# Kernel optimization log

Hardware: AMD Instinct MI355X
Metric: run time of the kernel (lower is better)

## Reference

```python
import jax, jax.numpy as jnp
import numpy as np

IGNORE_INDEX = -100


def setup_inputs() -> dict:
    key = jax.random.key(0)
    k1, k2, k3 = jax.random.split(key, 3)
    B, S, D, V = 2, 4096, 2048, 32000
    outputs = jax.random.normal(k1, (B, S, D), dtype=jnp.float32)
    # LM-head weight, nn.Linear convention: [vocab, embed_dim], scaled like typical init
    weight = jax.random.normal(k2, (V, D), dtype=jnp.float32) * (D ** -0.5)
    targets = jax.random.randint(k3, (B, S), 0, V, dtype=jnp.int64)
    return {"outputs": outputs, "weight": weight, "targets": targets}


def reference(outputs, weight, targets):
    # Flatten tokens: [B, S, D] -> [N, D], [B, S] -> [N]
    D = outputs.shape[-1]
    x = outputs.reshape(-1, D)            # [N, D]
    t = targets.reshape(-1)               # [N]
    # Fused linear projection: logits [N, V]
    logits = jnp.einsum("nd,vd->nv", x, weight)
    logp = jax.nn.log_softmax(logits, axis=-1)
    valid = t != IGNORE_INDEX
    safe_t = jnp.where(valid, t, 0)
    # Gather target log-prob per token
    nll = -jnp.take_along_axis(logp, safe_t[:, None], axis=1)[:, 0]  # [N]
    n_valid = jnp.maximum(jnp.sum(valid.astype(nll.dtype)), 1.0)
    loss = jnp.sum(jnp.where(valid, nll, 0.0)) / n_valid
    return loss
```

## Files before the change

kernel.cpp:

```cpp
#include <hip/hip_runtime.h>
#include <hip/hip_bf16.h>
#include <math.h>

#define IGNORE_INDEX (-100)

typedef __attribute__((ext_vector_type(4))) float f32x4;
typedef __attribute__((ext_vector_type(2))) long lx2;

static const int NTOK = 2 * 4096;
static const int DIM  = 2048;
static const int VOC  = 32000;
static const int BM = 256, BN = 256;
static const int KS = 64;
static const int NPH = DIM / KS;
static const int NVT = VOC / BN;
static const int MT  = NTOK / BM;
static const float WSCALE = 16.0f;


__device__ inline void gload_lds16(const void* g, void* l) {
  __builtin_amdgcn_global_load_lds(
      (const __attribute__((address_space(1))) void*)g,
      (__attribute__((address_space(3))) void*)l,
      16, 0, 0);
}


__global__ void cast_f32_fp8(const float* __restrict__ in,
                             unsigned char* __restrict__ out, long n8, float scale) {
  long i0 = (long)blockIdx.x * blockDim.x + threadIdx.x;
  long stride = (long)gridDim.x * blockDim.x;
  for (long i = i0; i < n8; i += stride) {
    const float4* p = (const float4*)(in + i * 8);
    float4 a = p[0], b = p[1];
    int lo = __builtin_amdgcn_cvt_pk_fp8_f32(a.x * scale, a.y * scale, 0, false);
    lo = __builtin_amdgcn_cvt_pk_fp8_f32(a.z * scale, a.w * scale, lo, true);
    int hi = __builtin_amdgcn_cvt_pk_fp8_f32(b.x * scale, b.y * scale, 0, false);
    hi = __builtin_amdgcn_cvt_pk_fp8_f32(b.z * scale, b.w * scale, hi, true);
    int2 o; o.x = lo; o.y = hi;
    *(int2*)(out + i * 8) = o;
  }
}


#define VM8  asm volatile("s_waitcnt vmcnt(8)" ::: "memory")
#define VM4  asm volatile("s_waitcnt vmcnt(4)" ::: "memory")
#define VM0  asm volatile("s_waitcnt vmcnt(0)" ::: "memory")
#define BARRIER asm volatile("s_barrier" ::: "memory")
#define LGKM0 asm volatile("s_waitcnt lgkmcnt(0)" ::: "memory")

#define MM2(ii, jj, AR, BR) do { \
  acc[ii][jj] = __builtin_amdgcn_mfma_f32_16x16x32_fp8_fp8(AR[0], BR[0], acc[ii][jj], 0, 0, 0); \
  acc[ii][jj] = __builtin_amdgcn_mfma_f32_16x16x32_fp8_fp8(AR[1], BR[1], acc[ii][jj], 0, 0, 0); \
} while (0)

__launch_bounds__(512, 2)
__global__ void lce_gemm(const unsigned char* __restrict__ xq,
                         const unsigned char* __restrict__ wq,
                         float* __restrict__ pmax, float* __restrict__ psum) {
  extern __shared__ char smem[];
  char* smA = smem;
  char* smB = smem + 65536;

  const int nwg = NVT * MT;
  const int cpx = nwg >> 3;
  const int bid = blockIdx.x;
  const int swz = (bid & 7) * cpx + (bid >> 3);
  const int vt = swz / MT;
  const int mt = swz % MT;
  const int m0 = mt * BM;
  const int v0 = vt * BN;

  const int tid = threadIdx.x;
  const int lane = tid & 63;
  const int w = tid >> 6;
  const int wr = w >> 2, wc = w & 3;
  const int li = lane & 15, lg = lane >> 4;

  f32x4 acc[8][4];
  const f32x4 z = {0.f, 0.f, 0.f, 0.f};
#pragma unroll
  for (int i = 0; i < 8; ++i)
#pragma unroll
    for (int j = 0; j < 4; ++j) acc[i][j] = z;

  const unsigned char* aS0 = xq + (long)(m0 + 2 * w * 16 + li) * DIM + lg * 16;
  const unsigned char* aS1 = xq + (long)(m0 + (2 * w + 1) * 16 + li) * DIM + lg * 16;
  const unsigned char* bS0 = wq + (long)(v0 + 2 * w * 16 + li) * DIM + lg * 16;
  const unsigned char* bS1 = wq + (long)(v0 + (2 * w + 1) * 16 + li) * DIM + lg * 16;
  char* stA = smA + 2 * w * 1024;
  char* stB = smB + 2 * w * 1024;

  const char* aRd = smA + wr * 8192 + lane * 16;
  const char* bRd = smB + wc * 4096 + lane * 16;

#pragma unroll
  for (int s = 0; s < 3; ++s) {
    gload_lds16(aS0, stA + s * 16384);        aS0 += KS;
    gload_lds16(aS1, stA + s * 16384 + 1024); aS1 += KS;
    gload_lds16(bS0, stB + s * 16384);        bS0 += KS;
    gload_lds16(bS1, stB + s * 16384 + 1024); bS1 += KS;
  }
  VM8;
  BARRIER;

#pragma unroll 1
  for (int n = 0; n < NPH; ++n) {
    const int slot = n & 3;
    const int dst = (n + 3) & 3;
    const char* Ab = aRd + slot * 16384;
    const char* Bb = bRd + slot * 16384;
    const bool stg = (n < NPH - 3);

    lx2 B0 = *(const lx2*)(Bb);
    lx2 B1 = *(const lx2*)(Bb + 1024);
    lx2 B2 = *(const lx2*)(Bb + 2048);
    lx2 B3 = *(const lx2*)(Bb + 3072);
    lx2 A0 = *(const lx2*)(Ab);
    lx2 A1 = *(const lx2*)(Ab + 1024);
    if (stg) { gload_lds16(aS0, stA + dst * 16384); aS0 += KS; }
    BARRIER; LGKM0;
    __builtin_amdgcn_s_setprio(1);
    MM2(0, 0, A0, B0); MM2(0, 1, A0, B1); MM2(0, 2, A0, B2); MM2(0, 3, A0, B3);
    MM2(1, 0, A1, B0); MM2(1, 1, A1, B1); MM2(1, 2, A1, B2); MM2(1, 3, A1, B3);
    __builtin_amdgcn_s_setprio(0);
    BARRIER;

    A0 = *(const lx2*)(Ab + 2048);
    A1 = *(const lx2*)(Ab + 3072);
    if (stg) { gload_lds16(aS1, stA + dst * 16384 + 1024); aS1 += KS; }
    BARRIER; LGKM0;
    __builtin_amdgcn_s_setprio(1);
    MM2(2, 0, A0, B0); MM2(2, 1, A0, B1); MM2(2, 2, A0, B2); MM2(2, 3, A0, B3);
    MM2(3, 0, A1, B0); MM2(3, 1, A1, B1); MM2(3, 2, A1, B2); MM2(3, 3, A1, B3);
    __builtin_amdgcn_s_setprio(0);
    BARRIER;

    A0 = *(const lx2*)(Ab + 4096);
    A1 = *(const lx2*)(Ab + 5120);
    if (stg) { gload_lds16(bS0, stB + dst * 16384); bS0 += KS; }
    BARRIER; LGKM0;
    __builtin_amdgcn_s_setprio(1);
    MM2(4, 0, A0, B0); MM2(4, 1, A0, B1); MM2(4, 2, A0, B2); MM2(4, 3, A0, B3);
    MM2(5, 0, A1, B0); MM2(5, 1, A1, B1); MM2(5, 2, A1, B2); MM2(5, 3, A1, B3);
    __builtin_amdgcn_s_setprio(0);
    BARRIER;

    A0 = *(const lx2*)(Ab + 6144);
    A1 = *(const lx2*)(Ab + 7168);
    if (stg) { gload_lds16(bS1, stB + dst * 16384 + 1024); bS1 += KS; }
    BARRIER; LGKM0;
    __builtin_amdgcn_s_setprio(1);
    MM2(6, 0, A0, B0); MM2(6, 1, A0, B1); MM2(6, 2, A0, B2); MM2(6, 3, A0, B3);
    MM2(7, 0, A1, B0); MM2(7, 1, A1, B1); MM2(7, 2, A1, B2); MM2(7, 3, A1, B3);
    __builtin_amdgcn_s_setprio(0);
    if (n < NPH - 3) { VM8; }
    else if (n == NPH - 3) { VM4; }
    else if (n == NPH - 2) { VM0; }
    BARRIER;
  }

  const float sc = 1.0f / WSCALE;
  float* sm_m = (float*)smem;
  float* sm_s = (float*)(smem + 4096);
  __syncthreads();
#pragma unroll
  for (int i = 0; i < 8; ++i) {
#pragma unroll
    for (int r = 0; r < 4; ++r) {
      float l0 = acc[i][0][r] * sc, l1 = acc[i][1][r] * sc;
      float l2 = acc[i][2][r] * sc, l3 = acc[i][3][r] * sc;
      float m = fmaxf(fmaxf(l0, l1), fmaxf(l2, l3));
#pragma unroll
      for (int mk = 1; mk < 16; mk <<= 1) m = fmaxf(m, __shfl_xor(m, mk));
      float s = __expf(l0 - m) + __expf(l1 - m) + __expf(l2 - m) + __expf(l3 - m);
#pragma unroll
      for (int mk = 1; mk < 16; mk <<= 1) s += __shfl_xor(s, mk);
      if (li == 0) {
        int R = wr * 128 + i * 16 + lg * 4 + r;
        sm_m[wc * 256 + R] = m;
        sm_s[wc * 256 + R] = s;
      }
    }
  }
  __syncthreads();
  if (tid < BM) {
    float ma = sm_m[tid], mb = sm_m[256 + tid], mc = sm_m[512 + tid], md = sm_m[768 + tid];
    float gm = fmaxf(fmaxf(ma, mb), fmaxf(mc, md));
    float gs = sm_s[tid] * __expf(ma - gm) + sm_s[256 + tid] * __expf(mb - gm) +
               sm_s[512 + tid] * __expf(mc - gm) + sm_s[768 + tid] * __expf(md - gm);
    long row = (long)(m0 + tid);
    pmax[row * NVT + vt] = gm;
    psum[row * NVT + vt] = gs;
  }
}


__global__ void token_reduce(const float* __restrict__ x, const float* __restrict__ wgt,
                             const int* __restrict__ tgt,
                             const float* __restrict__ pmax, const float* __restrict__ psum,
                             float* __restrict__ nll, float* __restrict__ validf) {
  const int n = blockIdx.x;
  const int tid = threadIdx.x;
  const int lane = tid & 63;
  const int w = tid >> 6;
  __shared__ float smr[4];

  const int t = tgt[n];
  const bool valid = (t != IGNORE_INDEX);
  const int ts = valid ? t : 0;

  const float4* xr = (const float4*)(x + (long)n * DIM);
  const float4* wr = (const float4*)(wgt + (long)ts * DIM);
  float d = 0.f;
  for (int i = tid; i < DIM / 4; i += blockDim.x) {
    float4 a = xr[i], b = wr[i];
    d += a.x * b.x + a.y * b.y + a.z * b.z + a.w * b.w;
  }

  float m = (tid < NVT) ? pmax[(long)n * NVT + tid] : -INFINITY;
  float t1 = m;
#pragma unroll
  for (int mk = 1; mk < 64; mk <<= 1) t1 = fmaxf(t1, __shfl_xor(t1, mk));
  if (lane == 0) smr[w] = t1;
  __syncthreads();
  const float gm = fmaxf(fmaxf(smr[0], smr[1]), fmaxf(smr[2], smr[3]));
  __syncthreads();

  float se = (tid < NVT) ? psum[(long)n * NVT + tid] * __expf(m - gm) : 0.f;
#pragma unroll
  for (int mk = 1; mk < 64; mk <<= 1) se += __shfl_xor(se, mk);
  if (lane == 0) smr[w] = se;
  __syncthreads();
  const float gs = smr[0] + smr[1] + smr[2] + smr[3];
  __syncthreads();

#pragma unroll
  for (int mk = 1; mk < 64; mk <<= 1) d += __shfl_xor(d, mk);
  if (lane == 0) smr[w] = d;
  __syncthreads();
  const float gd = smr[0] + smr[1] + smr[2] + smr[3];

  if (tid == 0) {
    nll[n] = valid ? (gm + logf(gs) - gd) : 0.f;
    validf[n] = valid ? 1.f : 0.f;
  }
}


__global__ void final_reduce(const float* __restrict__ nll, const float* __restrict__ validf,
                             float* __restrict__ out, int n) {
  const int tid = threadIdx.x;
  const int lane = tid & 63;
  const int w = tid >> 6;
  __shared__ float sm1[4], sm2[4];
  float s = 0.f, c = 0.f;
  for (int i = tid; i < n; i += blockDim.x) { s += nll[i]; c += validf[i]; }
#pragma unroll
  for (int mk = 1; mk < 64; mk <<= 1) { s += __shfl_xor(s, mk); c += __shfl_xor(c, mk); }
  if (lane == 0) { sm1[w] = s; sm2[w] = c; }
  __syncthreads();
  if (tid == 0) {
    float ts = sm1[0] + sm1[1] + sm1[2] + sm1[3];
    float tc = sm2[0] + sm2[1] + sm2[2] + sm2[3];
    out[0] = ts / fmaxf(tc, 1.0f);
  }
}


extern "C" void kernel_launch(void* const* d_in, const int* in_sizes, int n_in,
                              void* d_out, int out_size, void* d_ws, size_t ws_size,
                              hipStream_t stream) {
  const float* x = (const float*)d_in[0];
  const float* wgt = (const float*)d_in[1];
  const int* tgt = (const int*)d_in[2];
  float* out = (float*)d_out;

  char* ws = (char*)d_ws;
  const size_t xq_off = 0;
  const size_t wq_off = (size_t)NTOK * DIM;
  const size_t pm_off = wq_off + (size_t)VOC * DIM;
  const size_t ps_off = pm_off + (size_t)NTOK * NVT * 4;
  const size_t nl_off = ps_off + (size_t)NTOK * NVT * 4;
  const size_t vf_off = nl_off + (size_t)NTOK * 4;
  const size_t needed = vf_off + (size_t)NTOK * 4;
  if (ws_size < needed) return;

  unsigned char* xq = (unsigned char*)(ws + xq_off);
  unsigned char* wq = (unsigned char*)(ws + wq_off);
  float* pmax = (float*)(ws + pm_off);
  float* psum = (float*)(ws + ps_off);
  float* nllv = (float*)(ws + nl_off);
  float* vldf = (float*)(ws + vf_off);

  cast_f32_fp8<<<2048, 256, 0, stream>>>(x, xq, (long)NTOK * DIM / 8, 1.0f);
  cast_f32_fp8<<<4096, 256, 0, stream>>>(wgt, wq, (long)VOC * DIM / 8, WSCALE);

  (void)hipFuncSetAttribute((const void*)lce_gemm,
                            hipFuncAttributeMaxDynamicSharedMemorySize, 131072);
  lce_gemm<<<NVT * MT, 512, 131072, stream>>>(xq, wq, pmax, psum);

  token_reduce<<<NTOK, 256, 0, stream>>>(x, wgt, tgt, pmax, psum, nllv, vldf);
  final_reduce<<<1, 256, 0, stream>>>(nllv, vldf, out, NTOK);
}
```

Measured before the change: 959.9 us.

## Switch FP8 GEMM to 32x32x64 scaled MFMA with restructured tiling

Replaces the 16x16x32 FP8 MFMA pairs with the gfx950 mfma_scale_f32_32x32x64_f8f6f4 instruction using unit scales, and reorganises the LDS staging layout, per-wave fragment loads and accumulator shape (4x2 of 32x32 tiles) to match. The main loop now has two compute phases per K-step instead of four, so it issues fewer barriers and fewer, larger MFMAs. The softmax epilogue is remapped to the 32x32 output layout with 32-lane reductions. This risks layout or indexing mistakes in the new fragment mapping, and the staging barriers now group two global loads each.

```diff
diff --git a/kernel.cpp b/kernel.cpp
--- a/kernel.cpp
+++ b/kernel.cpp
@@ -5,7 +5,9 @@
 #define IGNORE_INDEX (-100)
 
 typedef __attribute__((ext_vector_type(4))) float f32x4;
-typedef __attribute__((ext_vector_type(2))) long lx2;
+typedef __attribute__((ext_vector_type(16))) float f32x16;
+typedef __attribute__((ext_vector_type(4))) int i32x4;
+typedef __attribute__((ext_vector_type(8))) int i32x8;
 
 static const int NTOK = 2 * 4096;
 static const int DIM  = 2048;
@@ -16,6 +18,7 @@
 static const int NVT = VOC / BN;
 static const int MT  = NTOK / BM;
 static const float WSCALE = 16.0f;
+#define SCL1 0x7F7F7F7F
 
 
 __device__ inline void gload_lds16(const void* g, void* l) {
@@ -49,10 +52,11 @@
 #define BARRIER asm volatile("s_barrier" ::: "memory")
 #define LGKM0 asm volatile("s_waitcnt lgkmcnt(0)" ::: "memory")
 
-#define MM2(ii, jj, AR, BR) do { \
-  acc[ii][jj] = __builtin_amdgcn_mfma_f32_16x16x32_fp8_fp8(AR[0], BR[0], acc[ii][jj], 0, 0, 0); \
-  acc[ii][jj] = __builtin_amdgcn_mfma_f32_16x16x32_fp8_fp8(AR[1], BR[1], acc[ii][jj], 0, 0, 0); \
-} while (0)
+#define MS(ACC, AV, BV) \
+  ACC = __builtin_amdgcn_mfma_scale_f32_32x32x64_f8f6f4( \
+      AV, BV, ACC, 0, 0, 0, SCL1, 0, SCL1)
+
+#define PACK8(LO, HI) {LO[0], LO[1], LO[2], LO[3], HI[0], HI[1], HI[2], HI[3]}
 
 __launch_bounds__(512, 2)
 __global__ void lce_gemm(const unsigned char* __restrict__ xq,
@@ -75,24 +79,26 @@
   const int lane = tid & 63;
   const int w = tid >> 6;
   const int wr = w >> 2, wc = w & 3;
-  const int li = lane & 15, lg = lane >> 4;
-
-  f32x4 acc[8][4];
-  const f32x4 z = {0.f, 0.f, 0.f, 0.f};
-#pragma unroll
-  for (int i = 0; i < 8; ++i)
-#pragma unroll
-    for (int j = 0; j < 4; ++j) acc[i][j] = z;
-
-  const unsigned char* aS0 = xq + (long)(m0 + 2 * w * 16 + li) * DIM + lg * 16;
-  const unsigned char* aS1 = xq + (long)(m0 + (2 * w + 1) * 16 + li) * DIM + lg * 16;
-  const unsigned char* bS0 = wq + (long)(v0 + 2 * w * 16 + li) * DIM + lg * 16;
-  const unsigned char* bS1 = wq + (long)(v0 + (2 * w + 1) * 16 + li) * DIM + lg * 16;
-  char* stA = smA + 2 * w * 1024;
-  char* stB = smB + 2 * w * 1024;
-
-  const char* aRd = smA + wr * 8192 + lane * 16;
-  const char* bRd = smB + wc * 4096 + lane * 16;
+  const int lc = lane & 31;
+  const int lh = lane >> 5;
+
+  f32x16 acc[4][2];
+#pragma unroll
+  for (int i = 0; i < 4; ++i)
+#pragma unroll
+    for (int j = 0; j < 2; ++j)
+#pragma unroll
+      for (int r = 0; r < 16; ++r) acc[i][j][r] = 0.f;
+
+  const unsigned char* aS0 = xq + (long)(m0 + w * 32 + lc) * DIM + lh * 32;
+  const unsigned char* aS1 = aS0 + 16;
+  const unsigned char* bS0 = wq + (long)(v0 + w * 32 + lc) * DIM + lh * 32;
+  const unsigned char* bS1 = bS0 + 16;
+  char* stA = smA + w * 2048;
+  char* stB = smB + w * 2048;
+
+  const char* aRd = smA + wr * 4 * 2048 + lane * 16;
+  const char* bRd = smB + wc * 2 * 2048 + lane * 16;
 
 #pragma unroll
   for (int s = 0; s < 3; ++s) {
@@ -112,48 +118,50 @@
     const char* Bb = bRd + slot * 16384;
     const bool stg = (n < NPH - 3);
 
-    lx2 B0 = *(const lx2*)(Bb);
-    lx2 B1 = *(const lx2*)(Bb + 1024);
-    lx2 B2 = *(const lx2*)(Bb + 2048);
-    lx2 B3 = *(const lx2*)(Bb + 3072);
-    lx2 A0 = *(const lx2*)(Ab);
-    lx2 A1 = *(const lx2*)(Ab + 1024);
-    if (stg) { gload_lds16(aS0, stA + dst * 16384); aS0 += KS; }
+    i32x4 b0l = *(const i32x4*)(Bb);
+    i32x4 b0h = *(const i32x4*)(Bb + 1024);
+    i32x4 b1l = *(const i32x4*)(Bb + 2048);
+    i32x4 b1h = *(const i32x4*)(Bb + 3072);
+    i32x4 a0l = *(const i32x4*)(Ab);
+    i32x4 a0h = *(const i32x4*)(Ab + 1024);
+    i32x4 a1l = *(const i32x4*)(Ab + 2048);
+    i32x4 a1h = *(const i32x4*)(Ab + 3072);
+    if (stg) {
+      gload_lds16(aS0, stA + dst * 16384);        aS0 += KS;
+      gload_lds16(aS1, stA + dst * 16384 + 1024); aS1 += KS;
+    }
     BARRIER; LGKM0;
-    __builtin_amdgcn_s_setprio(1);
-    MM2(0, 0, A0, B0); MM2(0, 1, A0, B1); MM2(0, 2, A0, B2); MM2(0, 3, A0, B3);
-    MM2(1, 0, A1, B0); MM2(1, 1, A1, B1); MM2(1, 2, A1, B2); MM2(1, 3, A1, B3);
-    __builtin_amdgcn_s_setprio(0);
+    {
+      i32x8 B0 = PACK8(b0l, b0h);
+      i32x8 B1 = PACK8(b1l, b1h);
+      i32x8 A0 = PACK8(a0l, a0h);
+      i32x8 A1 = PACK8(a1l, a1h);
+      __builtin_amdgcn_s_setprio(1);
+      MS(acc[0][0], A0, B0); MS(acc[0][1], A0, B1);
+      MS(acc[1][0], A1, B0); MS(acc[1][1], A1, B1);
+      __builtin_amdgcn_s_setprio(0);
+    }
     BARRIER;
 
-    A0 = *(const lx2*)(Ab + 2048);
-    A1 = *(const lx2*)(Ab + 3072);
-    if (stg) { gload_lds16(aS1, stA + dst * 16384 + 1024); aS1 += KS; }
+    i32x4 a2l = *(const i32x4*)(Ab + 4096);
+    i32x4 a2h = *(const i32x4*)(Ab + 5120);
+    i32x4 a3l = *(const i32x4*)(Ab + 6144);
+    i32x4 a3h = *(const i32x4*)(Ab + 7168);
+    if (stg) {
+      gload_lds16(bS0, stB + dst * 16384);        bS0 += KS;
+      gload_lds16(bS1, stB + dst * 16384 + 1024); bS1 += KS;
+    }
     BARRIER; LGKM0;
-    __builtin_amdgcn_s_setprio(1);
-    MM2(2, 0, A0, B0); MM2(2, 1, A0, B1); MM2(2, 2, A0, B2); MM2(2, 3, A0, B3);
-    MM2(3, 0, A1, B0); MM2(3, 1, A1, B1); MM2(3, 2, A1, B2); MM2(3, 3, A1, B3);
-    __builtin_amdgcn_s_setprio(0);
-    BARRIER;
-
-    A0 = *(const lx2*)(Ab + 4096);
-    A1 = *(const lx2*)(Ab + 5120);
-    if (stg) { gload_lds16(bS0, stB + dst * 16384); bS0 += KS; }
-    BARRIER; LGKM0;
-    __builtin_amdgcn_s_setprio(1);
-    MM2(4, 0, A0, B0); MM2(4, 1, A0, B1); MM2(4, 2, A0, B2); MM2(4, 3, A0, B3);
-    MM2(5, 0, A1, B0); MM2(5, 1, A1, B1); MM2(5, 2, A1, B2); MM2(5, 3, A1, B3);
-    __builtin_amdgcn_s_setprio(0);
-    BARRIER;
-
-    A0 = *(const lx2*)(Ab + 6144);
-    A1 = *(const lx2*)(Ab + 7168);
-    if (stg) { gload_lds16(bS1, stB + dst * 16384 + 1024); bS1 += KS; }
-    BARRIER; LGKM0;
-    __builtin_amdgcn_s_setprio(1);
-    MM2(6, 0, A0, B0); MM2(6, 1, A0, B1); MM2(6, 2, A0, B2); MM2(6, 3, A0, B3);
-    MM2(7, 0, A1, B0); MM2(7, 1, A1, B1); MM2(7, 2, A1, B2); MM2(7, 3, A1, B3);
-    __builtin_amdgcn_s_setprio(0);
+    {
+      i32x8 B0 = PACK8(b0l, b0h);
+      i32x8 B1 = PACK8(b1l, b1h);
+      i32x8 A2 = PACK8(a2l, a2h);
+      i32x8 A3 = PACK8(a3l, a3h);
+      __builtin_amdgcn_s_setprio(1);
+      MS(acc[2][0], A2, B0); MS(acc[2][1], A2, B1);
+      MS(acc[3][0], A3, B0); MS(acc[3][1], A3, B1);
+      __builtin_amdgcn_s_setprio(0);
+    }
     if (n < NPH - 3) { VM8; }
     else if (n == NPH - 3) { VM4; }
     else if (n == NPH - 2) { VM0; }
@@ -165,19 +173,18 @@
   float* sm_s = (float*)(smem + 4096);
   __syncthreads();
 #pragma unroll
-  for (int i = 0; i < 8; ++i) {
-#pragma unroll
-    for (int r = 0; r < 4; ++r) {
+  for (int i = 0; i < 4; ++i) {
+#pragma unroll
+    for (int r = 0; r < 16; ++r) {
       float l0 = acc[i][0][r] * sc, l1 = acc[i][1][r] * sc;
-      float l2 = acc[i][2][r] * sc, l3 = acc[i][3][r] * sc;
-      float m = fmaxf(fmaxf(l0, l1), fmaxf(l2, l3));
-#pragma unroll
-      for (int mk = 1; mk < 16; mk <<= 1) m = fmaxf(m, __shfl_xor(m, mk));
-      float s = __expf(l0 - m) + __expf(l1 - m) + __expf(l2 - m) + __expf(l3 - m);
-#pragma unroll
-      for (int mk = 1; mk < 16; mk <<= 1) s += __shfl_xor(s, mk);
-      if (li == 0) {
-        int R = wr * 128 + i * 16 + lg * 4 + r;
+      float m = fmaxf(l0, l1);
+#pragma unroll
+      for (int mk = 1; mk < 32; mk <<= 1) m = fmaxf(m, __shfl_xor(m, mk));
+      float s = __expf(l0 - m) + __expf(l1 - m);
+#pragma unroll
+      for (int mk = 1; mk < 32; mk <<= 1) s += __shfl_xor(s, mk);
+      if (lc == 0) {
+        int R = wr * 128 + i * 32 + (r & 3) + 8 * (r >> 2) + 4 * lh;
         sm_m[wc * 256 + R] = m;
         sm_s[wc * 256 + R] = s;
       }
```

New measurement: 1.060 ms. +10.5%, slower.
